# Kernel tuning notes

Measured on AMD Instinct MI355X. Metric: run time of the kernel, lower is better.

## Reference

```python
import jax, jax.numpy as jnp
import numpy as np

B, S, DIM = 2, 1024, 1024
E, K, INTER = 16, 2, 512
SHARED_INTER = 2 * INTER  # n_shared_experts * moe_inter_dim
ROUTE_SCALE = 1.0


def setup_inputs() -> dict:
    key = jax.random.key(0)
    ks = jax.random.split(key, 8)
    init = lambda k, shape: jax.random.normal(k, shape, dtype=jnp.float32) * 0.02
    return {
        "x": jax.random.normal(ks[0], (B, S, DIM), dtype=jnp.float32),
        "gate_w": init(ks[1], (E, DIM)),
        "w1": init(ks[2], (E, INTER, DIM)),
        "w2": init(ks[3], (E, DIM, INTER)),
        "w3": init(ks[4], (E, INTER, DIM)),
        "sw1": init(ks[5], (SHARED_INTER, DIM)),
        "sw2": init(ks[6], (DIM, SHARED_INTER)),
        "sw3": init(ks[7], (SHARED_INTER, DIM)),
    }


def reference(x, gate_w, w1, w2, w3, sw1, sw2, sw3):
    b, s, d = x.shape
    xt = x.reshape(-1, d)            # [T, D] flattened tokens
    T = xt.shape[0]

    # Gate: sigmoid scores, top-k experts, normalize selected weights
    scores = jax.nn.sigmoid(xt @ gate_w.T)           # [T, E]
    topv, topi = jax.lax.top_k(scores, K)            # [T, K]
    weights = topv / jnp.sum(topv, axis=-1, keepdims=True) * ROUTE_SCALE

    # Per-token dense combine weights over experts: gate[t, e]
    gate = jnp.zeros((T, E), xt.dtype).at[jnp.arange(T)[:, None], topi].add(weights)

    # Routed experts (SwiGLU), computed densely and combined with gate weights
    h = jax.nn.silu(jnp.einsum('td,eid->tei', xt, w1)) * jnp.einsum('td,eid->tei', xt, w3)
    expert_out = jnp.einsum('tei,edi->ted', h, w2)   # [T, E, D]
    y = jnp.einsum('ted,te->td', expert_out, gate)   # [T, D]

    # Shared expert (SwiGLU MLP over all tokens)
    z = (jax.nn.silu(xt @ sw1.T) * (xt @ sw3.T)) @ sw2.T

    return (y + z).reshape(b, s, d)
```

## Files before the change

### kernel.cpp

```cpp
#include <hip/hip_runtime.h>
#include <stdint.h>

typedef unsigned short u16;
typedef __bf16 bf16x8 __attribute__((ext_vector_type(8)));
typedef float f32x4 __attribute__((ext_vector_type(4)));
typedef unsigned short u16x8 __attribute__((ext_vector_type(8)));

#define TTOK 2048
#define DIMSZ 1024
#define NROUT 16
#define INTERSZ 512
#define BK 128
#define CHK 16

__device__ __forceinline__ u16 f2bf(float f) {
    unsigned int u = __builtin_bit_cast(unsigned int, f);
    unsigned int r = u + 0x7FFFu + ((u >> 16) & 1u);
    return (u16)(r >> 16);
}

__device__ __forceinline__ ushort4 cvt4(float4 a) {
    ushort4 o;
    o.x = f2bf(a.x); o.y = f2bf(a.y); o.z = f2bf(a.z); o.w = f2bf(a.w);
    return o;
}

__device__ __forceinline__ void gl2lds16(const void* g, void* l) {
    __builtin_amdgcn_global_load_lds(
        (const __attribute__((address_space(1))) void*)(uintptr_t)g,
        (__attribute__((address_space(3))) void*)(uintptr_t)l,
        16, 0, 0);
}

#define NF4A (NROUT * INTERSZ * DIMSZ / 4)
#define CASTA_BLKS 1024
#define CAST_BLKS 1152
#define SW2_BLKS 128
__global__ __launch_bounds__(256) void prep(
    const float* __restrict__ w1, const float* __restrict__ sw1,
    const float* __restrict__ w3, const float* __restrict__ sw3,
    const float* __restrict__ sw2,
    u16* __restrict__ W1b, u16* __restrict__ W3b, u16* __restrict__ W2sb,
    const float* __restrict__ x, const float* __restrict__ gw,
    int* __restrict__ topi, float2* __restrict__ topw,
    u16* __restrict__ Xbf) {
    const int r = blockIdx.y;
    const int tid = threadIdx.x;
    if (r < 3) {
        const float4* src; ushort4* dst;
        if (r < 2) {
            if (blockIdx.x >= CAST_BLKS) return;
            const float* a = r ? w3 : w1;
            const float* b = r ? sw3 : sw1;
            dst = (ushort4*)(r ? W3b : W1b);
            src = (blockIdx.x < CASTA_BLKS)
                  ? (const float4*)a
                  : (const float4*)b - (size_t)CASTA_BLKS * 2048;
        } else {
            if (blockIdx.x >= SW2_BLKS) return;
            src = (const float4*)sw2;
            dst = (ushort4*)W2sb;
        }
        const size_t gbase = (size_t)blockIdx.x * 2048;
        float4 v[8];
        #pragma unroll
        for (int k = 0; k < 8; ++k)
            v[k] = src[gbase + k * 256 + tid];
        #pragma unroll
        for (int k = 0; k < 8; ++k)
            dst[gbase + k * 256 + tid] = cvt4(v[k]);
        return;
    }
    const int t = blockIdx.x;
    const int wave = tid >> 6, lane = tid & 63;
    const int d0 = tid * 4;
    float4 xv = *(const float4*)(x + (size_t)t * DIMSZ + d0);
    *(ushort4*)&Xbf[(size_t)t * DIMSZ + d0] = cvt4(xv);

    float acc[16];
    #pragma unroll
    for (int e = 0; e < 16; ++e) {
        float4 g = *(const float4*)(gw + e * DIMSZ + d0);
        acc[e] = xv.x * g.x + xv.y * g.y + xv.z * g.z + xv.w * g.w;
    }
    #pragma unroll
    for (int off = 32; off > 0; off >>= 1) {
        #pragma unroll
        for (int e = 0; e < 16; ++e) acc[e] += __shfl_xor(acc[e], off);
    }
    __shared__ float part[4][16];
    __shared__ float sfin[16];
    if (lane < 16) part[wave][lane] = acc[lane];
    __syncthreads();
    if (wave == 0 && lane < 16) {
        float s = part[0][lane] + part[1][lane] + part[2][lane] + part[3][lane];
        sfin[lane] = 1.f / (1.f + expf(-s));
    }
    __syncthreads();
    if (tid == 0) {
        int i0 = 0; float v0 = sfin[0];
        #pragma unroll
        for (int e = 1; e < 16; ++e) { float v = sfin[e]; if (v > v0) { v0 = v; i0 = e; } }
        int i1 = -1; float v1 = -1e30f;
        #pragma unroll
        for (int e = 0; e < 16; ++e) { float v = sfin[e]; if (e != i0 && v > v1) { v1 = v; i1 = e; } }
        float inv = 1.f / (v0 + v1);
        topi[t] = i0 | (i1 << 8);
        topw[t] = make_float2(v0 * inv, v1 * inv);
    }
}

__global__ __launch_bounds__(256) void route_kernel(
    const int* __restrict__ topi, const float2* __restrict__ topw,
    int* __restrict__ counts, int* __restrict__ tokidx, float* __restrict__ tokw) {
    const int e = blockIdx.x;
    const int tid = threadIdx.x;
    int p[8]; int m[8]; int cnt = 0;
    #pragma unroll
    for (int j = 0; j < 8; ++j) {
        int t = tid * 8 + j;
        p[j] = topi[t];
        m[j] = ((p[j] & 255) == e) || ((p[j] >> 8) == e) ? 1 : 0;
        cnt += m[j];
    }
    const int lane = tid & 63, wave = tid >> 6;
    int v = cnt;
    #pragma unroll
    for (int off = 1; off < 64; off <<= 1) {
        int u = __shfl_up(v, off);
        if (lane >= off) v += u;
    }
    __shared__ int wsum[4];
    if (lane == 63) wsum[wave] = v;
    __syncthreads();
    int wbase = 0;
    #pragma unroll
    for (int w = 0; w < 4; ++w) wbase += (w < wave) ? wsum[w] : 0;
    int base = wbase + v - cnt;
    #pragma unroll
    for (int j = 0; j < 8; ++j) {
        if (m[j]) {
            int t = tid * 8 + j;
            float2 w2 = topw[t];
            tokidx[e * TTOK + base] = t;
            tokw[e * TTOK + base] = ((p[j] & 255) == e) ? w2.x : w2.y;
            ++base;
        }
    }
    if (tid == 0) counts[e] = wsum[0] + wsum[1] + wsum[2] + wsum[3];
}

__global__ __launch_bounds__(256) void gemm1s(
    const u16* __restrict__ Xbf, const u16* __restrict__ W1b,
    const u16* __restrict__ W3b, const int* __restrict__ counts,
    const int* __restrict__ tokidx, const float* __restrict__ tokw,
    u16* __restrict__ Hc, u16* __restrict__ Hs) {
    const int e = blockIdx.z;
    const int cnt = (e < NROUT) ? counts[e] : TTOK;
    const int m0 = blockIdx.y * 64;
    if (m0 >= cnt) return;
    const int n0 = blockIdx.x * 64;
    __shared__ u16 As[64 * BK], B1s[64 * BK], B3s[64 * BK];
    const u16* B1 = W1b + ((size_t)e * INTERSZ + n0) * DIMSZ;
    const u16* B3 = W3b + ((size_t)e * INTERSZ + n0) * DIMSZ;
    const int tid = threadIdx.x;

    int row[4], cgs[4]; size_t arow[4];
    #pragma unroll
    for (int i = 0; i < 4; ++i) {
        int c = tid + i * 256;
        row[i] = c >> 4;
        cgs[i] = ((c & 15) ^ (row[i] & 7)) * 8;
        int slot = m0 + row[i];
        int g;
        if (e < NROUT) g = (slot < cnt) ? tokidx[e * TTOK + slot] : 0;
        else           g = slot;
        arow[i] = (size_t)g * DIMSZ;
    }
    f32x4 acc1[2][2] = {}; f32x4 acc3[2][2] = {};
    const int wave = tid >> 6, lane = tid & 63;
    const int wm = (wave >> 1) * 32, wn = (wave & 1) * 32;
    const int lr = lane & 15, lq = lane >> 4;

    for (int kt = 0; kt < DIMSZ / BK; ++kt) {
        const int k0 = kt * BK;
        #pragma unroll
        for (int i = 0; i < 4; ++i) {
            int c = tid + i * 256;
            gl2lds16(Xbf + arow[i] + k0 + cgs[i], &As[c * 8]);
            size_t boff = (size_t)row[i] * DIMSZ + k0 + cgs[i];
            gl2lds16(B1 + boff, &B1s[c * 8]);
            gl2lds16(B3 + boff, &B3s[c * 8]);
        }
        __syncthreads();
        #pragma unroll
        for (int ks = 0; ks < 4; ++ks) {
            bf16x8 af[2], b1f[2], b3f[2];
            const int g = ks * 4 + lq;
            #pragma unroll
            for (int mt = 0; mt < 2; ++mt) {
                int m = wm + mt * 16 + lr;
                af[mt] = *(const bf16x8*)&As[(m * CHK + (g ^ (m & 7))) * 8];
            }
            #pragma unroll
            for (int nt = 0; nt < 2; ++nt) {
                int n = wn + nt * 16 + lr;
                int ch = (n * CHK + (g ^ (n & 7))) * 8;
                b1f[nt] = *(const bf16x8*)&B1s[ch];
                b3f[nt] = *(const bf16x8*)&B3s[ch];
            }
            #pragma unroll
            for (int mt = 0; mt < 2; ++mt) {
                #pragma unroll
                for (int nt = 0; nt < 2; ++nt) {
                    acc1[mt][nt] = __builtin_amdgcn_mfma_f32_16x16x32_bf16(af[mt], b1f[nt], acc1[mt][nt], 0, 0, 0);
                    acc3[mt][nt] = __builtin_amdgcn_mfma_f32_16x16x32_bf16(af[mt], b3f[nt], acc3[mt][nt], 0, 0, 0);
                }
            }
        }
        __syncthreads();
    }
    #pragma unroll
    for (int mt = 0; mt < 2; ++mt) {
        #pragma unroll
        for (int nt = 0; nt < 2; ++nt) {
            #pragma unroll
            for (int r = 0; r < 4; ++r) {
                int m = wm + mt * 16 + lq * 4 + r;
                int n = wn + nt * 16 + lr;
                int slot = m0 + m;
                bool valid = slot < cnt;
                float h1 = acc1[mt][nt][r], h3 = acc3[mt][nt][r];
                float hv = 0.f;
                if (valid) {
                    float tw = (e < NROUT) ? tokw[e * TTOK + slot] : 1.0f;
                    hv = h1 / (1.f + __expf(-h1)) * h3 * tw;
                }
                if (e < NROUT)
                    Hc[((size_t)e * TTOK + slot) * INTERSZ + n0 + n] = f2bf(hv);
                else
                    Hs[(size_t)slot * DIMSZ + (e - NROUT) * INTERSZ + n0 + n] = f2bf(hv);
            }
        }
    }
}

__global__ __launch_bounds__(256) void gemm2rt(
    const u16* __restrict__ Hc, const float* __restrict__ w2f,
    const int* __restrict__ counts, const int* __restrict__ tokidx,
    const int* __restrict__ topi,
    float* __restrict__ bufA, float* __restrict__ bufB) {
    const int e = blockIdx.y;
    const int n0 = blockIdx.x * 32;
    const int cnt = counts[e];
    const int tid = threadIdx.x;
    __shared__ u16 Bs[32 * INTERSZ];
    __shared__ u16 As[64 * BK];

    const float4* B0 = (const float4*)(w2f + ((size_t)e * DIMSZ + n0) * INTERSZ);
    #pragma unroll
    for (int it2 = 0; it2 < 2; ++it2) {
        float4 v[8];
        #pragma unroll
        for (int k = 0; k < 8; ++k)
            v[k] = B0[(it2 * 8 + k) * 256 + tid];
        #pragma unroll
        for (int k = 0; k < 8; ++k) {
            int q = (it2 * 8 + k) * 256 + tid;
            int brow = q >> 7;
            int c = (q & 127) >> 1;
            int h = q & 1;
            *(ushort4*)&Bs[((brow << 6) + (c ^ (brow & 7))) * 8 + h * 4] = cvt4(v[k]);
        }
    }
    __syncthreads();

    const int wave = tid >> 6, lane = tid & 63;
    const int wm = (wave >> 1) * 32, wn = (wave & 1) * 16;
    const int lr = lane & 15, lq = lane >> 4;
    int row[4], cgs[4];
    #pragma unroll
    for (int i = 0; i < 4; ++i) {
        int c = tid + i * 256;
        row[i] = c >> 4;
        cgs[i] = ((c & 15) ^ (row[i] & 7)) * 8;
    }

    for (int m0 = 0; m0 < cnt; m0 += 64) {
        const u16* A0 = Hc + ((size_t)e * TTOK + m0) * INTERSZ;
        f32x4 acc[2] = {};
        for (int kt = 0; kt < INTERSZ / BK; ++kt) {
            const int k0 = kt * BK;
            #pragma unroll
            for (int i = 0; i < 4; ++i) {
                int c = tid + i * 256;
                gl2lds16(A0 + (size_t)row[i] * INTERSZ + k0 + cgs[i], &As[c * 8]);
            }
            __syncthreads();
            #pragma unroll
            for (int ks = 0; ks < 4; ++ks) {
                bf16x8 af[2], bfr;
                const int g = ks * 4 + lq;
                #pragma unroll
                for (int mt = 0; mt < 2; ++mt) {
                    int m = wm + mt * 16 + lr;
                    af[mt] = *(const bf16x8*)&As[(m * CHK + (g ^ (m & 7))) * 8];
                }
                {
                    int n = wn + lr;
                    bfr = *(const bf16x8*)&Bs[(n * 64 + kt * CHK + (g ^ (n & 7))) * 8];
                }
                #pragma unroll
                for (int mt = 0; mt < 2; ++mt) {
                    acc[mt] = __builtin_amdgcn_mfma_f32_16x16x32_bf16(af[mt], bfr, acc[mt], 0, 0, 0);
                }
            }
            __syncthreads();
        }
        #pragma unroll
        for (int mt = 0; mt < 2; ++mt) {
            #pragma unroll
            for (int r = 0; r < 4; ++r) {
                int m = wm + mt * 16 + lq * 4 + r;
                int slot = m0 + m;
                if (slot < cnt) {
                    int t = tokidx[e * TTOK + slot];
                    float* db = ((topi[t] & 255) == e) ? bufA : bufB;
                    int n = wn + lr;
                    db[(size_t)t * DIMSZ + n0 + n] = acc[mt][r];
                }
            }
        }
    }
}

__global__ __launch_bounds__(256) void gemm2sh(
    const u16* __restrict__ Hs, const u16* __restrict__ W2sb,
    const float* __restrict__ bufA, const float* __restrict__ bufB,
    float* __restrict__ out) {
    const int m0 = blockIdx.y * 64;
    const int n0 = blockIdx.x * 64;
    __shared__ u16 As[64 * BK], Bs[64 * BK];
    const u16* A0 = Hs + (size_t)m0 * DIMSZ;
    const u16* B0 = W2sb + (size_t)n0 * DIMSZ;
    const int tid = threadIdx.x;
    const int wave = tid >> 6, lane = tid & 63;
    const int wm = (wave >> 1) * 32, wn = (wave & 1) * 32;
    const int lr = lane & 15, lq = lane >> 4;

    int row[4], cgs[4];
    #pragma unroll
    for (int i = 0; i < 4; ++i) {
        int c = tid + i * 256;
        row[i] = c >> 4;
        cgs[i] = ((c & 15) ^ (row[i] & 7)) * 8;
    }

    f32x4 acc[2][2] = {};
    for (int kt = 0; kt < DIMSZ / BK; ++kt) {
        const int k0 = kt * BK;
        #pragma unroll
        for (int i = 0; i < 4; ++i) {
            int c = tid + i * 256;
            gl2lds16(A0 + (size_t)row[i] * DIMSZ + k0 + cgs[i], &As[c * 8]);
            gl2lds16(B0 + (size_t)row[i] * DIMSZ + k0 + cgs[i], &Bs[c * 8]);
        }
        __syncthreads();
        #pragma unroll
        for (int ks = 0; ks < 4; ++ks) {
            bf16x8 af[2], bfr[2];
            const int g = ks * 4 + lq;
            #pragma unroll
            for (int mt = 0; mt < 2; ++mt) {
                int m = wm + mt * 16 + lr;
                af[mt] = *(const bf16x8*)&As[(m * CHK + (g ^ (m & 7))) * 8];
            }
            #pragma unroll
            for (int nt = 0; nt < 2; ++nt) {
                int n = wn + nt * 16 + lr;
                bfr[nt] = *(const bf16x8*)&Bs[(n * CHK + (g ^ (n & 7))) * 8];
            }
            #pragma unroll
            for (int mt = 0; mt < 2; ++mt) {
                #pragma unroll
                for (int nt = 0; nt < 2; ++nt) {
                    acc[mt][nt] = __builtin_amdgcn_mfma_f32_16x16x32_bf16(af[mt], bfr[nt], acc[mt][nt], 0, 0, 0);
                }
            }
        }
        __syncthreads();
    }
    #pragma unroll
    for (int mt = 0; mt < 2; ++mt) {
        #pragma unroll
        for (int r = 0; r < 4; ++r) {
            int t = m0 + wm + mt * 16 + lq * 4 + r;
            #pragma unroll
            for (int nt = 0; nt < 2; ++nt) {
                int n = wn + nt * 16 + lr;
                size_t idx = (size_t)t * DIMSZ + n0 + n;
                out[idx] = acc[mt][nt][r] + bufA[idx] + bufB[idx];
            }
        }
    }
}

extern "C" void kernel_launch(void* const* d_in, const int* in_sizes, int n_in,
                              void* d_out, int out_size, void* d_ws, size_t ws_size,
                              hipStream_t stream) {
    const float* x      = (const float*)d_in[0];
    const float* gate_w = (const float*)d_in[1];
    const float* w1     = (const float*)d_in[2];
    const float* w2     = (const float*)d_in[3];
    const float* w3     = (const float*)d_in[4];
    const float* sw1    = (const float*)d_in[5];
    const float* sw2    = (const float*)d_in[6];
    const float* sw3    = (const float*)d_in[7];
    float* out = (float*)d_out;

    char* ws = (char*)d_ws;
    const size_t SZ_W   = (size_t)(NROUT + 2) * INTERSZ * DIMSZ * 2;
    const size_t SZ_XBF = (size_t)TTOK * DIMSZ * 2;
    u16*   W1b    = (u16*)(ws);
    u16*   W3b    = (u16*)(ws + SZ_W);
    u16*   W2all  = (u16*)(ws + 2 * SZ_W);
    u16*   Xbf    = (u16*)(ws + 3 * SZ_W);
    char*  route  = ws + 3 * SZ_W + SZ_XBF;
    int*   counts = (int*)route;
    int*   topi   = (int*)(route + 256);
    float2* topw  = (float2*)(route + 256 + TTOK * 4);
    int*   tokidx = (int*)(route + 256 + TTOK * 12);
    float* tokw   = (float*)(route + 256 + TTOK * 12 + 16 * TTOK * 4);
    char*  hbuf   = route + 256 + TTOK * 12 + 2 * (size_t)16 * TTOK * 4;
    u16*   Hc     = (u16*)hbuf;
    u16*   Hs     = (u16*)(hbuf + (size_t)NROUT * TTOK * INTERSZ * 2);
    char*  bufs   = hbuf + (size_t)NROUT * TTOK * INTERSZ * 2 + (size_t)TTOK * DIMSZ * 2;
    float* bufA   = (float*)bufs;
    float* bufB   = (float*)(bufs + (size_t)TTOK * DIMSZ * 4);
    u16*   W2sb   = W2all + (size_t)NROUT * DIMSZ * INTERSZ;

    prep<<<dim3(2048, 4), 256, 0, stream>>>(
        w1, sw1, w3, sw3, sw2, W1b, W3b, W2sb,
        x, gate_w, topi, topw, Xbf);
    route_kernel<<<NROUT, 256, 0, stream>>>(topi, topw, counts, tokidx, tokw);
    gemm1s<<<dim3(INTERSZ / 64, TTOK / 64, NROUT + 2), 256, 0, stream>>>(
        Xbf, W1b, W3b, counts, tokidx, tokw, Hc, Hs);
    gemm2rt<<<dim3(DIMSZ / 32, NROUT), 256, 0, stream>>>(
        Hc, w2, counts, tokidx, topi, bufA, bufB);
    gemm2sh<<<dim3(DIMSZ / 64, TTOK / 64), 256, 0, stream>>>(
        Hs, W2sb, bufA, bufB, out);
}
```

Measured before the change: 238.2 us.

## Remap GEMM block indices per XCD so each expert stays on one die

Flattens the gemm1s and gemm2rt grids to 1D and decodes block ids so blocks of the same expert land on the same XCD (id & 7), which should improve L2 reuse of that expert's weights. It also splits the monolithic prep kernel into two cast launches plus a gate/sw2 kernel, removing the early-exit idle blocks of the 2D prep grid. The cost is extra kernel launches, and the XCD mapping assumes round-robin block dispatch across 8 XCDs.

```diff
diff --git a/kernel.cpp b/kernel.cpp
--- a/kernel.cpp
+++ b/kernel.cpp
@@ -32,35 +32,34 @@
         16, 0, 0);
 }
 
-#define NF4A (NROUT * INTERSZ * DIMSZ / 4)
 #define CASTA_BLKS 1024
-#define CAST_BLKS 1152
-#define SW2_BLKS 128
-__global__ __launch_bounds__(256) void prep(
-    const float* __restrict__ w1, const float* __restrict__ sw1,
-    const float* __restrict__ w3, const float* __restrict__ sw3,
-    const float* __restrict__ sw2,
-    u16* __restrict__ W1b, u16* __restrict__ W3b, u16* __restrict__ W2sb,
+__global__ __launch_bounds__(256) void cast6(
+    const float* __restrict__ a, const float* __restrict__ b,
+    u16* __restrict__ d) {
+    const int tid = threadIdx.x;
+    const float4* src = (blockIdx.x < CASTA_BLKS)
+                        ? (const float4*)a
+                        : (const float4*)b - (size_t)CASTA_BLKS * 2048;
+    ushort4* dst = (ushort4*)d;
+    const size_t gbase = (size_t)blockIdx.x * 2048;
+    float4 v[8];
+    #pragma unroll
+    for (int k = 0; k < 8; ++k)
+        v[k] = src[gbase + k * 256 + tid];
+    #pragma unroll
+    for (int k = 0; k < 8; ++k)
+        dst[gbase + k * 256 + tid] = cvt4(v[k]);
+}
+
+__global__ __launch_bounds__(256) void gatep(
+    const float* __restrict__ sw2, u16* __restrict__ W2sb,
     const float* __restrict__ x, const float* __restrict__ gw,
     int* __restrict__ topi, float2* __restrict__ topw,
     u16* __restrict__ Xbf) {
-    const int r = blockIdx.y;
-    const int tid = threadIdx.x;
-    if (r < 3) {
-        const float4* src; ushort4* dst;
-        if (r < 2) {
-            if (blockIdx.x >= CAST_BLKS) return;
-            const float* a = r ? w3 : w1;
-            const float* b = r ? sw3 : sw1;
-            dst = (ushort4*)(r ? W3b : W1b);
-            src = (blockIdx.x < CASTA_BLKS)
-                  ? (const float4*)a
-                  : (const float4*)b - (size_t)CASTA_BLKS * 2048;
-        } else {
-            if (blockIdx.x >= SW2_BLKS) return;
-            src = (const float4*)sw2;
-            dst = (ushort4*)W2sb;
-        }
+    const int tid = threadIdx.x;
+    if (blockIdx.x < 128) {
+        const float4* src = (const float4*)sw2;
+        ushort4* dst = (ushort4*)W2sb;
         const size_t gbase = (size_t)blockIdx.x * 2048;
         float4 v[8];
         #pragma unroll
@@ -71,7 +70,7 @@
             dst[gbase + k * 256 + tid] = cvt4(v[k]);
         return;
     }
-    const int t = blockIdx.x;
+    const int t = blockIdx.x - 128;
     const int wave = tid >> 6, lane = tid & 63;
     const int d0 = tid * 4;
     float4 xv = *(const float4*)(x + (size_t)t * DIMSZ + d0);
@@ -155,11 +154,24 @@
     const u16* __restrict__ W3b, const int* __restrict__ counts,
     const int* __restrict__ tokidx, const float* __restrict__ tokw,
     u16* __restrict__ Hc, u16* __restrict__ Hs) {
-    const int e = blockIdx.z;
+    int e, n0, m0;
+    {
+        const int id = blockIdx.x;
+        if (id < 4096) {
+            const int xcd = id & 7, q = id >> 3;
+            e = xcd + 8 * (q >> 8);
+            const int k = q & 255;
+            n0 = (k >> 5) * 64; m0 = (k & 31) * 64;
+        } else {
+            const int id2 = id - 4096;
+            const int xcd = id2 & 7, q = id2 >> 3;
+            const int s = xcd + 8 * (q >> 5);
+            e = NROUT + (s >> 3);
+            n0 = (s & 7) * 64; m0 = (q & 31) * 64;
+        }
+    }
     const int cnt = (e < NROUT) ? counts[e] : TTOK;
-    const int m0 = blockIdx.y * 64;
     if (m0 >= cnt) return;
-    const int n0 = blockIdx.x * 64;
     __shared__ u16 As[64 * BK], B1s[64 * BK], B3s[64 * BK];
     const u16* B1 = W1b + ((size_t)e * INTERSZ + n0) * DIMSZ;
     const u16* B3 = W3b + ((size_t)e * INTERSZ + n0) * DIMSZ;
@@ -250,8 +262,10 @@
     const int* __restrict__ counts, const int* __restrict__ tokidx,
     const int* __restrict__ topi,
     float* __restrict__ bufA, float* __restrict__ bufB) {
-    const int e = blockIdx.y;
-    const int n0 = blockIdx.x * 32;
+    const int id = blockIdx.x;
+    const int xcd = id & 7, q = id >> 3;
+    const int e = xcd + 8 * (q >> 5);
+    const int n0 = (q & 31) * 32;
     const int cnt = counts[e];
     const int tid = threadIdx.x;
     __shared__ u16 Bs[32 * INTERSZ];
@@ -266,10 +280,10 @@
             v[k] = B0[(it2 * 8 + k) * 256 + tid];
         #pragma unroll
         for (int k = 0; k < 8; ++k) {
-            int q = (it2 * 8 + k) * 256 + tid;
-            int brow = q >> 7;
-            int c = (q & 127) >> 1;
-            int h = q & 1;
+            int qq = (it2 * 8 + k) * 256 + tid;
+            int brow = qq >> 7;
+            int c = (qq & 127) >> 1;
+            int h = qq & 1;
             *(ushort4*)&Bs[((brow << 6) + (c ^ (brow & 7))) * 8 + h * 4] = cvt4(v[k]);
         }
     }
@@ -439,13 +453,14 @@
     float* bufB   = (float*)(bufs + (size_t)TTOK * DIMSZ * 4);
     u16*   W2sb   = W2all + (size_t)NROUT * DIMSZ * INTERSZ;
 
-    prep<<<dim3(2048, 4), 256, 0, stream>>>(
-        w1, sw1, w3, sw3, sw2, W1b, W3b, W2sb,
-        x, gate_w, topi, topw, Xbf);
+    cast6<<<dim3(1152), 256, 0, stream>>>(w1, sw1, W1b);
+    cast6<<<dim3(1152), 256, 0, stream>>>(w3, sw3, W3b);
+    gatep<<<dim3(2048 + 128), 256, 0, stream>>>(
+        sw2, W2sb, x, gate_w, topi, topw, Xbf);
     route_kernel<<<NROUT, 256, 0, stream>>>(topi, topw, counts, tokidx, tokw);
-    gemm1s<<<dim3(INTERSZ / 64, TTOK / 64, NROUT + 2), 256, 0, stream>>>(
+    gemm1s<<<dim3(4608), 256, 0, stream>>>(
         Xbf, W1b, W3b, counts, tokidx, tokw, Hc, Hs);
-    gemm2rt<<<dim3(DIMSZ / 32, NROUT), 256, 0, stream>>>(
+    gemm2rt<<<dim3(512), 256, 0, stream>>>(
         Hc, w2, counts, tokidx, topi, bufA, bufB);
     gemm2sh<<<dim3(DIMSZ / 64, TTOK / 64), 256, 0, stream>>>(
         Hs, W2sb, bufA, bufB, out);
```

Result: slower. 243.7 us (+2.3%).

## Fuse MoE stages into cooperative persistent kernel with atomic output accumulation

Applied to the files above, without the earlier changes.

Merges the prep, routing, gemm1 and gemm2 stages into one cooperative persistent kernel whose phases are separated by grid-wide syncs, with a multi-kernel fallback. The intermediate bufA/bufB buffers and the final combine pass are replaced by zeroing the output during the gate phase and accumulating routed and shared expert results with float atomics. This targets launch overhead and a full-size extra read/write pass over the output, in exchange for grid.sync costs, occupancy limited to three blocks per CU, and atomic contention. Atomic float adds also make the summation order nondeterministic.

```diff
diff --git a/kernel.cpp b/kernel.cpp
--- a/kernel.cpp
+++ b/kernel.cpp
@@ -1,10 +1,12 @@
 #include <hip/hip_runtime.h>
+#include <hip/hip_cooperative_groups.h>
 #include <stdint.h>
+
+namespace cg = cooperative_groups;
 
 typedef unsigned short u16;
 typedef __bf16 bf16x8 __attribute__((ext_vector_type(8)));
 typedef float f32x4 __attribute__((ext_vector_type(4)));
-typedef unsigned short u16x8 __attribute__((ext_vector_type(8)));
 
 #define TTOK 2048
 #define DIMSZ 1024
@@ -12,6 +14,7 @@
 #define INTERSZ 512
 #define BK 128
 #define CHK 16
+#define SMEM_BYTES 49152
 
 __device__ __forceinline__ u16 f2bf(float f) {
     unsigned int u = __builtin_bit_cast(unsigned int, f);
@@ -32,48 +35,44 @@
         16, 0, 0);
 }
 
-#define NF4A (NROUT * INTERSZ * DIMSZ / 4)
-#define CASTA_BLKS 1024
-#define CAST_BLKS 1152
-#define SW2_BLKS 128
-__global__ __launch_bounds__(256) void prep(
+
+__device__ __forceinline__ void cast_unit(
+    int u, int tid,
     const float* __restrict__ w1, const float* __restrict__ sw1,
     const float* __restrict__ w3, const float* __restrict__ sw3,
     const float* __restrict__ sw2,
-    u16* __restrict__ W1b, u16* __restrict__ W3b, u16* __restrict__ W2sb,
+    u16* __restrict__ W1b, u16* __restrict__ W3b, u16* __restrict__ W2sb) {
+    const float4* src; ushort4* dst; size_t gbase;
+    if (u < 1152) {
+        src = (u < 1024) ? (const float4*)w1
+                         : (const float4*)sw1 - (size_t)1024 * 2048;
+        dst = (ushort4*)W1b; gbase = (size_t)u * 2048;
+    } else if (u < 2304) {
+        int b = u - 1152;
+        src = (b < 1024) ? (const float4*)w3
+                         : (const float4*)sw3 - (size_t)1024 * 2048;
+        dst = (ushort4*)W3b; gbase = (size_t)b * 2048;
+    } else {
+        int b = u - 2304;
+        src = (const float4*)sw2; dst = (ushort4*)W2sb; gbase = (size_t)b * 2048;
+    }
+    float4 v[8];
+    #pragma unroll
+    for (int k = 0; k < 8; ++k) v[k] = src[gbase + k * 256 + tid];
+    #pragma unroll
+    for (int k = 0; k < 8; ++k) dst[gbase + k * 256 + tid] = cvt4(v[k]);
+}
+
+__device__ __forceinline__ void gate_unit(
+    int t, int tid, char* smem,
     const float* __restrict__ x, const float* __restrict__ gw,
     int* __restrict__ topi, float2* __restrict__ topw,
-    u16* __restrict__ Xbf) {
-    const int r = blockIdx.y;
-    const int tid = threadIdx.x;
-    if (r < 3) {
-        const float4* src; ushort4* dst;
-        if (r < 2) {
-            if (blockIdx.x >= CAST_BLKS) return;
-            const float* a = r ? w3 : w1;
-            const float* b = r ? sw3 : sw1;
-            dst = (ushort4*)(r ? W3b : W1b);
-            src = (blockIdx.x < CASTA_BLKS)
-                  ? (const float4*)a
-                  : (const float4*)b - (size_t)CASTA_BLKS * 2048;
-        } else {
-            if (blockIdx.x >= SW2_BLKS) return;
-            src = (const float4*)sw2;
-            dst = (ushort4*)W2sb;
-        }
-        const size_t gbase = (size_t)blockIdx.x * 2048;
-        float4 v[8];
-        #pragma unroll
-        for (int k = 0; k < 8; ++k)
-            v[k] = src[gbase + k * 256 + tid];
-        #pragma unroll
-        for (int k = 0; k < 8; ++k)
-            dst[gbase + k * 256 + tid] = cvt4(v[k]);
-        return;
-    }
-    const int t = blockIdx.x;
+    u16* __restrict__ Xbf, float* __restrict__ out) {
+    float* part = (float*)smem;
+    float* sfin = (float*)(smem + 256);
     const int wave = tid >> 6, lane = tid & 63;
     const int d0 = tid * 4;
+    *(float4*)(out + (size_t)t * DIMSZ + d0) = make_float4(0.f, 0.f, 0.f, 0.f);
     float4 xv = *(const float4*)(x + (size_t)t * DIMSZ + d0);
     *(ushort4*)&Xbf[(size_t)t * DIMSZ + d0] = cvt4(xv);
 
@@ -88,12 +87,10 @@
         #pragma unroll
         for (int e = 0; e < 16; ++e) acc[e] += __shfl_xor(acc[e], off);
     }
-    __shared__ float part[4][16];
-    __shared__ float sfin[16];
-    if (lane < 16) part[wave][lane] = acc[lane];
+    if (lane < 16) part[wave * 16 + lane] = acc[lane];
     __syncthreads();
     if (wave == 0 && lane < 16) {
-        float s = part[0][lane] + part[1][lane] + part[2][lane] + part[3][lane];
+        float s = part[lane] + part[16 + lane] + part[32 + lane] + part[48 + lane];
         sfin[lane] = 1.f / (1.f + expf(-s));
     }
     __syncthreads();
@@ -108,13 +105,14 @@
         topi[t] = i0 | (i1 << 8);
         topw[t] = make_float2(v0 * inv, v1 * inv);
     }
-}
-
-__global__ __launch_bounds__(256) void route_kernel(
+    __syncthreads();
+}
+
+__device__ __forceinline__ void route_body(
+    int e, int tid, char* smem,
     const int* __restrict__ topi, const float2* __restrict__ topw,
     int* __restrict__ counts, int* __restrict__ tokidx, float* __restrict__ tokw) {
-    const int e = blockIdx.x;
-    const int tid = threadIdx.x;
+    int* wsum = (int*)smem;
     int p[8]; int m[8]; int cnt = 0;
     #pragma unroll
     for (int j = 0; j < 8; ++j) {
@@ -130,7 +128,6 @@
         int u = __shfl_up(v, off);
         if (lane >= off) v += u;
     }
-    __shared__ int wsum[4];
     if (lane == 63) wsum[wave] = v;
     __syncthreads();
     int wbase = 0;
@@ -150,20 +147,28 @@
     if (tid == 0) counts[e] = wsum[0] + wsum[1] + wsum[2] + wsum[3];
 }
 
-__global__ __launch_bounds__(256) void gemm1s(
+__device__ __forceinline__ void gemm1_tile(
+    int id, int tid, char* smem,
     const u16* __restrict__ Xbf, const u16* __restrict__ W1b,
     const u16* __restrict__ W3b, const int* __restrict__ counts,
     const int* __restrict__ tokidx, const float* __restrict__ tokw,
     u16* __restrict__ Hc, u16* __restrict__ Hs) {
-    const int e = blockIdx.z;
+    int e, n0, m0;
+    if (id < 4096) {
+        e = id >> 8; int r2 = id & 255;
+        n0 = (r2 >> 5) * 64; m0 = (r2 & 31) * 64;
+    } else {
+        int id2 = id - 4096;
+        e = NROUT + (id2 >> 8); int r2 = id2 & 255;
+        n0 = (r2 >> 5) * 64; m0 = (r2 & 31) * 64;
+    }
     const int cnt = (e < NROUT) ? counts[e] : TTOK;
-    const int m0 = blockIdx.y * 64;
     if (m0 >= cnt) return;
-    const int n0 = blockIdx.x * 64;
-    __shared__ u16 As[64 * BK], B1s[64 * BK], B3s[64 * BK];
+    u16* As  = (u16*)smem;
+    u16* B1s = (u16*)(smem + 16384);
+    u16* B3s = (u16*)(smem + 32768);
     const u16* B1 = W1b + ((size_t)e * INTERSZ + n0) * DIMSZ;
     const u16* B3 = W3b + ((size_t)e * INTERSZ + n0) * DIMSZ;
-    const int tid = threadIdx.x;
 
     int row[4], cgs[4]; size_t arow[4];
     #pragma unroll
@@ -245,17 +250,16 @@
     }
 }
 
-__global__ __launch_bounds__(256) void gemm2rt(
+__device__ __forceinline__ void g2rt_tile(
+    int u, int tid, char* smem,
     const u16* __restrict__ Hc, const float* __restrict__ w2f,
     const int* __restrict__ counts, const int* __restrict__ tokidx,
-    const int* __restrict__ topi,
-    float* __restrict__ bufA, float* __restrict__ bufB) {
-    const int e = blockIdx.y;
-    const int n0 = blockIdx.x * 32;
+    float* __restrict__ out) {
+    const int e = u >> 5;
+    const int n0 = (u & 31) * 32;
     const int cnt = counts[e];
-    const int tid = threadIdx.x;
-    __shared__ u16 Bs[32 * INTERSZ];
-    __shared__ u16 As[64 * BK];
+    u16* Bs = (u16*)smem;
+    u16* As = (u16*)(smem + 32768);
 
     const float4* B0 = (const float4*)(w2f + ((size_t)e * DIMSZ + n0) * INTERSZ);
     #pragma unroll
@@ -266,10 +270,10 @@
             v[k] = B0[(it2 * 8 + k) * 256 + tid];
         #pragma unroll
         for (int k = 0; k < 8; ++k) {
-            int q = (it2 * 8 + k) * 256 + tid;
-            int brow = q >> 7;
-            int c = (q & 127) >> 1;
-            int h = q & 1;
+            int qq = (it2 * 8 + k) * 256 + tid;
+            int brow = qq >> 7;
+            int c = (qq & 127) >> 1;
+            int h = qq & 1;
             *(ushort4*)&Bs[((brow << 6) + (c ^ (brow & 7))) * 8 + h * 4] = cvt4(v[k]);
         }
     }
@@ -325,25 +329,24 @@
                 int slot = m0 + m;
                 if (slot < cnt) {
                     int t = tokidx[e * TTOK + slot];
-                    float* db = ((topi[t] & 255) == e) ? bufA : bufB;
                     int n = wn + lr;
-                    db[(size_t)t * DIMSZ + n0 + n] = acc[mt][r];
-                }
-            }
-        }
-    }
-}
-
-__global__ __launch_bounds__(256) void gemm2sh(
+                    unsafeAtomicAdd(&out[(size_t)t * DIMSZ + n0 + n], acc[mt][r]);
+                }
+            }
+        }
+    }
+}
+
+__device__ __forceinline__ void g2sh_tile(
+    int u, int tid, char* smem,
     const u16* __restrict__ Hs, const u16* __restrict__ W2sb,
-    const float* __restrict__ bufA, const float* __restrict__ bufB,
     float* __restrict__ out) {
-    const int m0 = blockIdx.y * 64;
-    const int n0 = blockIdx.x * 64;
-    __shared__ u16 As[64 * BK], Bs[64 * BK];
+    const int m0 = (u >> 4) * 64;
+    const int n0 = (u & 15) * 64;
+    u16* As = (u16*)smem;
+    u16* Bs = (u16*)(smem + 16384);
     const u16* A0 = Hs + (size_t)m0 * DIMSZ;
     const u16* B0 = W2sb + (size_t)n0 * DIMSZ;
-    const int tid = threadIdx.x;
     const int wave = tid >> 6, lane = tid & 63;
     const int wm = (wave >> 1) * 32, wn = (wave & 1) * 32;
     const int lr = lane & 15, lq = lane >> 4;
@@ -398,10 +401,85 @@
             #pragma unroll
             for (int nt = 0; nt < 2; ++nt) {
                 int n = wn + nt * 16 + lr;
-                size_t idx = (size_t)t * DIMSZ + n0 + n;
-                out[idx] = acc[mt][nt][r] + bufA[idx] + bufB[idx];
-            }
-        }
+                unsafeAtomicAdd(&out[(size_t)t * DIMSZ + n0 + n], acc[mt][nt][r]);
+            }
+        }
+    }
+}
+
+__global__ __launch_bounds__(256, 3) void mega(
+    const float* __restrict__ x, const float* __restrict__ gw,
+    const float* __restrict__ w1, const float* __restrict__ w3,
+    const float* __restrict__ sw1, const float* __restrict__ sw3,
+    const float* __restrict__ sw2, const float* __restrict__ w2f,
+    u16* __restrict__ W1b, u16* __restrict__ W3b, u16* __restrict__ W2sb,
+    u16* __restrict__ Xbf, int* __restrict__ topi, float2* __restrict__ topw,
+    int* __restrict__ counts, int* __restrict__ tokidx, float* __restrict__ tokw,
+    u16* __restrict__ Hc, u16* __restrict__ Hs, float* __restrict__ out) {
+    cg::grid_group grid = cg::this_grid();
+    const int tid = threadIdx.x;
+    const int nb = gridDim.x;
+    __shared__ char smem[SMEM_BYTES];
+
+    for (int u = blockIdx.x; u < 2432 + TTOK; u += nb) {
+        if (u < 2432) cast_unit(u, tid, w1, sw1, w3, sw3, sw2, W1b, W3b, W2sb);
+        else          gate_unit(u - 2432, tid, smem, x, gw, topi, topw, Xbf, out);
+    }
+    __threadfence(); grid.sync(); __threadfence();
+
+    if (blockIdx.x < NROUT)
+        route_body(blockIdx.x, tid, smem, topi, topw, counts, tokidx, tokw);
+    __threadfence(); grid.sync(); __threadfence();
+
+    for (int u = blockIdx.x; u < 4608; u += nb)
+        gemm1_tile(u, tid, smem, Xbf, W1b, W3b, counts, tokidx, tokw, Hc, Hs);
+    __threadfence(); grid.sync(); __threadfence();
+
+    for (int u = blockIdx.x; u < 1024; u += nb) {
+        if (u < 512) g2rt_tile(u, tid, smem, Hc, w2f, counts, tokidx, out);
+        else         g2sh_tile(u - 512, tid, smem, Hs, W2sb, out);
+    }
+}
+
+__global__ __launch_bounds__(256, 3) void p1k(
+    const float* __restrict__ x, const float* __restrict__ gw,
+    const float* __restrict__ w1, const float* __restrict__ w3,
+    const float* __restrict__ sw1, const float* __restrict__ sw3,
+    const float* __restrict__ sw2,
+    u16* __restrict__ W1b, u16* __restrict__ W3b, u16* __restrict__ W2sb,
+    u16* __restrict__ Xbf, int* __restrict__ topi, float2* __restrict__ topw,
+    float* __restrict__ out) {
+    __shared__ char smem[512];
+    const int tid = threadIdx.x;
+    for (int u = blockIdx.x; u < 2432 + TTOK; u += gridDim.x) {
+        if (u < 2432) cast_unit(u, tid, w1, sw1, w3, sw3, sw2, W1b, W3b, W2sb);
+        else          gate_unit(u - 2432, tid, smem, x, gw, topi, topw, Xbf, out);
+    }
+}
+__global__ __launch_bounds__(256) void p2k(
+    const int* __restrict__ topi, const float2* __restrict__ topw,
+    int* __restrict__ counts, int* __restrict__ tokidx, float* __restrict__ tokw) {
+    __shared__ char smem[64];
+    route_body(blockIdx.x, threadIdx.x, smem, topi, topw, counts, tokidx, tokw);
+}
+__global__ __launch_bounds__(256, 3) void p3k(
+    const u16* __restrict__ Xbf, const u16* __restrict__ W1b,
+    const u16* __restrict__ W3b, const int* __restrict__ counts,
+    const int* __restrict__ tokidx, const float* __restrict__ tokw,
+    u16* __restrict__ Hc, u16* __restrict__ Hs) {
+    __shared__ char smem[SMEM_BYTES];
+    for (int u = blockIdx.x; u < 4608; u += gridDim.x)
+        gemm1_tile(u, threadIdx.x, smem, Xbf, W1b, W3b, counts, tokidx, tokw, Hc, Hs);
+}
+__global__ __launch_bounds__(256, 3) void p4k(
+    const u16* __restrict__ Hc, const float* __restrict__ w2f,
+    const u16* __restrict__ Hs, const u16* __restrict__ W2sb,
+    const int* __restrict__ counts, const int* __restrict__ tokidx,
+    float* __restrict__ out) {
+    __shared__ char smem[SMEM_BYTES];
+    for (int u = blockIdx.x; u < 1024; u += gridDim.x) {
+        if (u < 512) g2rt_tile(u, threadIdx.x, smem, Hc, w2f, counts, tokidx, out);
+        else         g2sh_tile(u - 512, threadIdx.x, smem, Hs, W2sb, out);
     }
 }
 
@@ -434,19 +512,35 @@
     char*  hbuf   = route + 256 + TTOK * 12 + 2 * (size_t)16 * TTOK * 4;
     u16*   Hc     = (u16*)hbuf;
     u16*   Hs     = (u16*)(hbuf + (size_t)NROUT * TTOK * INTERSZ * 2);
-    char*  bufs   = hbuf + (size_t)NROUT * TTOK * INTERSZ * 2 + (size_t)TTOK * DIMSZ * 2;
-    float* bufA   = (float*)bufs;
-    float* bufB   = (float*)(bufs + (size_t)TTOK * DIMSZ * 4);
     u16*   W2sb   = W2all + (size_t)NROUT * DIMSZ * INTERSZ;
 
-    prep<<<dim3(2048, 4), 256, 0, stream>>>(
-        w1, sw1, w3, sw3, sw2, W1b, W3b, W2sb,
-        x, gate_w, topi, topw, Xbf);
-    route_kernel<<<NROUT, 256, 0, stream>>>(topi, topw, counts, tokidx, tokw);
-    gemm1s<<<dim3(INTERSZ / 64, TTOK / 64, NROUT + 2), 256, 0, stream>>>(
-        Xbf, W1b, W3b, counts, tokidx, tokw, Hc, Hs);
-    gemm2rt<<<dim3(DIMSZ / 32, NROUT), 256, 0, stream>>>(
-        Hc, w2, counts, tokidx, topi, bufA, bufB);
-    gemm2sh<<<dim3(DIMSZ / 64, TTOK / 64), 256, 0, stream>>>(
-        Hs, W2sb, bufA, bufB, out);
-}
+    int maxb = 0;
+    hipError_t qe = hipOccupancyMaxActiveBlocksPerMultiprocessor(
+        &maxb, reinterpret_cast<const void*>(mega), 256, 0);
+    bool done = false;
+    if (qe == hipSuccess && maxb >= 1) {
+        int nblk = maxb * 256;
+        if (nblk > 4480) nblk = 4480;
+        void* args[] = {
+            (void*)&x, (void*)&gate_w, (void*)&w1, (void*)&w3,
+            (void*)&sw1, (void*)&sw3, (void*)&sw2, (void*)&w2,
+            (void*)&W1b, (void*)&W3b, (void*)&W2sb,
+            (void*)&Xbf, (void*)&topi, (void*)&topw,
+            (void*)&counts, (void*)&tokidx, (void*)&tokw,
+            (void*)&Hc, (void*)&Hs, (void*)&out };
+        hipError_t le = hipLaunchCooperativeKernel(
+            reinterpret_cast<const void*>(mega), dim3(nblk), dim3(256),
+            args, 0, stream);
+        done = (le == hipSuccess);
+    }
+    if (!done) {
+        p1k<<<dim3(768), 256, 0, stream>>>(
+            x, gate_w, w1, w3, sw1, sw3, sw2, W1b, W3b, W2sb,
+            Xbf, topi, topw, out);
+        p2k<<<dim3(NROUT), 256, 0, stream>>>(topi, topw, counts, tokidx, tokw);
+        p3k<<<dim3(4608), 256, 0, stream>>>(
+            Xbf, W1b, W3b, counts, tokidx, tokw, Hc, Hs);
+        p4k<<<dim3(1024), 256, 0, stream>>>(
+            Hc, w2, Hs, W2sb, counts, tokidx, out);
+    }
+}
```

Result: slower. 690.4 us (+189.9%).
